# Performance work log

Measured on AMD Instinct MI355X. Metric: run time of the kernel, lower is better.

## Reference

```python
import jax, jax.numpy as jnp
import numpy as np

B, L, D = 8, 8192, 1024
M = L // 4  # target_ratio=4 -> exactly L/4 boundaries per batch row (enforced in setup_inputs)


@jax.custom_vjp
def ste(x):
    # Forward: ones_like(x). Backward: pass gradient straight through.
    return jnp.ones_like(x)

def _ste_fwd(x):
    return jnp.ones_like(x), None

def _ste_bwd(_, g):
    return (g,)

ste.defvjp(_ste_fwd, _ste_bwd)


def _ema_combine(c1, c2):
    # Linear recurrence h = a*h_prev + b as an associative op (matches the
    # Hillis-Steele doubling scan in the torch source exactly).
    a1, b1 = c1
    a2, b2 = c2
    return (a1 * a2, a2[..., None] * b1 + b2)


def setup_inputs() -> dict:
    key = jax.random.key(0)
    k1, k2, k3, k4, k5 = jax.random.split(key, 5)
    x = jax.random.normal(k1, (B, L, D), jnp.float32)
    residual = jax.random.normal(k2, (B, L, D), jnp.float32)
    prob = jax.random.uniform(k3, (B, L), jnp.float32)
    # exactly M=L//4 True positions per row (random locations) -> static M
    r = jax.random.uniform(k4, (B, L))
    sel = jnp.argsort(r, axis=1)[:, :M]
    token_mask = jnp.zeros((B, L), bool).at[jnp.arange(B)[:, None], sel].set(True)
    state = jax.random.normal(k5, (B, D), jnp.float32)
    return {"x": x, "residual": residual, "prob": prob,
            "token_mask": token_mask, "state": state}


def reference(x, residual, prob, token_mask, state):
    # ---- Tokenizer: compact selected positions to the front (stable order) ----
    counts = token_mask.sum(axis=1)                       # (B,)
    order = jnp.argsort(~token_mask, axis=1)[:, :M]       # stable: True positions first, in order
    chunked = jnp.take_along_axis(x, order[:, :, None], axis=1)      # (B, M, D)
    chunk_probs = jnp.take_along_axis(prob, order, axis=1)           # (B, M)
    valid = jnp.arange(M)[None, :] < counts[:, None]                  # (B, M)
    chunk_probs = chunk_probs * valid                     # padded slots -> 0 (new_zeros semantics)

    # ---- EMA scan over compacted chunks ----
    decay = jnp.clip(1.0 - chunk_probs, 0.0, 1.0)         # (B, M)
    b = (1.0 - decay)[..., None] * chunked                # (B, M, D)
    b = b.at[:, 0].add(decay[:, 0, None] * state)         # fold initial state into b[0]
    _, ema = jax.lax.associative_scan(_ema_combine, (decay, b), axis=1)
    ema = ema * valid[..., None]

    # ---- DeTokenizer: scatter-expand back to (B, L, D) ----
    chunk_idx = jnp.cumsum(token_mask.astype(jnp.int32), axis=1) - 1  # (B, L)
    valid_pos = chunk_idx >= 0
    ci = jnp.clip(chunk_idx, 0, M - 1)
    long_states = jnp.take_along_axis(ema, ci[:, :, None], axis=1)    # (B, L, D)
    long_states = long_states * valid_pos[..., None]

    coef = ste(jnp.maximum(1.0 - prob, prob))             # forward: ones; bwd: STE
    long_states = long_states * coef[..., None]

    output = residual + long_states                       # (B, L, D)

    # new_state = last valid EMA value per batch (or carried-over state if empty)
    last = jnp.clip(counts - 1, 0, M - 1)
    new_state = jnp.take_along_axis(ema, last[:, None, None], axis=1)[:, 0]
    new_state = jnp.where((counts > 0)[:, None], new_state, state)
    return output, new_state
```

## Files before the change

kernel.cpp:

```cpp
#include <hip/hip_runtime.h>
#include <stdint.h>
#include <stddef.h>

#define B_ 8
#define L_ 8192
#define D_ 1024
#define M_ 2048
#define S_ 128
#define G_ 16
#define D4_ (D_/4)
#define TROWS_ 64
#define NTILE_ (L_/TROWS_)

typedef float f4 __attribute__((ext_vector_type(4)));

#define OFF_POS    ((size_t)0)
#define OFF_DEC    (OFF_POS  + (size_t)B_*M_*4)
#define OFF_A      (OFF_DEC  + (size_t)B_*M_*4)
#define OFF_CIT    (OFF_A    + (size_t)B_*S_*4)
#define OFF_EZ     (OFF_CIT  + (size_t)B_*NTILE_*4)
#define OFF_HINIT  (OFF_EZ   + (size_t)B_*S_*D_*4)
#define WS_TOTAL   (OFF_HINIT + (size_t)B_*S_*D_*4)

__global__ __launch_bounds__(1024)
void compact_kernel(const void* __restrict__ mask_raw,
                    const float* __restrict__ prob,
                    int* __restrict__ pos,
                    float* __restrict__ dec,
                    int* __restrict__ ci_tile) {
    const int b = blockIdx.x;
    const int t = threadIdx.x;

    __shared__ int u8flag;
    if (t == 0) u8flag = 0;
    __syncthreads();
    {
        const uint32_t* mu = (const uint32_t*)mask_raw;
        uint32_t w0 = mu[t * 2], w1 = mu[t * 2 + 1];
        if (w0 > 1u || w1 > 1u) atomicOr(&u8flag, 1);
    }
    __syncthreads();
    const bool u8 = (u8flag != 0);

    int mv[8];
    const int base_l = t * 8;
    if (u8) {
        const uint8_t* mrow = (const uint8_t*)mask_raw + (size_t)b * L_;
        #pragma unroll
        for (int j = 0; j < 8; j++) mv[j] = mrow[base_l + j] ? 1 : 0;
    } else {
        const int* mrow = (const int*)mask_raw + (size_t)b * L_;
        #pragma unroll
        for (int j = 0; j < 8; j++) mv[j] = mrow[base_l + j] ? 1 : 0;
    }
    int tsum = 0;
    #pragma unroll
    for (int j = 0; j < 8; j++) tsum += mv[j];

    const int lane = t & 63, wid = t >> 6;
    int v = tsum;
    #pragma unroll
    for (int off = 1; off < 64; off <<= 1) {
        int n = __shfl_up(v, off, 64);
        if (lane >= off) v += n;
    }
    __shared__ int wsum[16];
    __shared__ int woff[16];
    if (lane == 63) wsum[wid] = v;
    __syncthreads();
    if (t < 16) {
        int acc = 0;
        for (int w = 0; w < t; w++) acc += wsum[w];
        woff[t] = acc;
    }
    __syncthreads();
    int run = (v - tsum) + woff[wid];

    const float* prow = prob + (size_t)b * L_;
    #pragma unroll
    for (int j = 0; j < 8; j++) {
        const int l = base_l + j;
        if (mv[j]) {
            float d = 1.0f - prow[l];
            d = fminf(fmaxf(d, 0.0f), 1.0f);
            pos[(size_t)b * M_ + run] = l;
            dec[(size_t)b * M_ + run] = d;
            run += 1;
        }
    }
    if ((t & 7) == 7) {
        const int k = (t + 1) >> 3;
        if (k < NTILE_) ci_tile[b * NTILE_ + k] = run - 1;
    }
}

__global__ __launch_bounds__(256)
void segend_kernel(const f4* __restrict__ x4,
                   const int* __restrict__ pos,
                   const float* __restrict__ dec,
                   f4* __restrict__ ez4,
                   float* __restrict__ Aseg) {
    const int blk = blockIdx.x;
    const int b = blk / S_, s = blk % S_;
    const int t = threadIdx.x;
    __shared__ int   pl[G_];
    __shared__ float dl[G_];
    if (t < G_) {
        pl[t] = pos[(size_t)b * M_ + (size_t)s * G_ + t];
        dl[t] = dec[(size_t)b * M_ + (size_t)s * G_ + t];
    }
    __syncthreads();
    f4 h = (f4)(0.0f);
    #pragma unroll
    for (int m = 0; m < G_; m++) {
        const float d = dl[m];
        h = d * h + (1.0f - d) * x4[((size_t)b * L_ + pl[m]) * D4_ + t];
    }
    ez4[(size_t)blk * D4_ + t] = h;
    if (t == 0) {
        float p = 1.0f;
        #pragma unroll
        for (int m = 0; m < G_; m++) p *= dl[m];
        Aseg[blk] = p;
    }
}

__global__ __launch_bounds__(64)
void combine_kernel(const float* __restrict__ ez,
                    const float* __restrict__ Aseg,
                    const float* __restrict__ state,
                    float* __restrict__ hinit,
                    float* __restrict__ newstate) {
    const int b = blockIdx.x;
    const int ch = blockIdx.y * 64 + threadIdx.x;
    __shared__ float Al[S_];
    for (int i = threadIdx.x; i < S_; i += 64) Al[i] = Aseg[b * S_ + i];
    __syncthreads();

    float c = state[(size_t)b * D_ + ch];
    for (int s0 = 0; s0 < S_; s0 += 8) {
        float e[8];
        #pragma unroll
        for (int j = 0; j < 8; j++)
            e[j] = ez[((size_t)b * S_ + s0 + j) * D_ + ch];
        #pragma unroll
        for (int j = 0; j < 8; j++) {
            hinit[((size_t)b * S_ + s0 + j) * D_ + ch] = c;
            c = fmaf(Al[s0 + j], c, e[j]);
        }
    }
    newstate[(size_t)b * D_ + ch] = c;
}

__global__ __launch_bounds__(256)
void fused_kernel(const f4* __restrict__ x4,
                  const f4* __restrict__ res4,
                  const int* __restrict__ pos,
                  const float* __restrict__ dec,
                  const int* __restrict__ ci_tile,
                  const float* __restrict__ state,
                  const f4* __restrict__ hinit4,
                  f4* __restrict__ out4) {
    const int blk = blockIdx.x;
    const int b = blk >> 7;
    const int k = blk & (NTILE_ - 1);
    const int t = threadIdx.x;
    const int l0 = k * TROWS_;

    const int m0 = (k == 0) ? -1 : ci_tile[b * NTILE_ + k];

    __shared__ int   pl[TROWS_ + 2];
    __shared__ float dl[TROWS_ + 2];
    if (t < TROWS_ + 2) {
        const int mm = m0 + 1 + t;
        if (mm < M_) {
            pl[t] = pos[(size_t)b * M_ + mm];
            dl[t] = dec[(size_t)b * M_ + mm];
        } else {
            pl[t] = L_;
            dl[t] = 1.0f;
        }
    }
    __syncthreads();

    const f4* xrow = x4 + (size_t)b * L_ * D4_;

    f4 h;
    float live;
    if (m0 < 0) {
        h = ((const f4*)state)[(size_t)b * D4_ + t];
        live = 0.0f;
    } else {
        const int s0 = m0 >> 4;
        const int mbase = s0 << 4;
        h = hinit4[((size_t)b * S_ + s0) * D4_ + t];
        live = 1.0f;
        #pragma unroll
        for (int j = 0; j < G_; j++) {
            const int mj = mbase + j;
            const float draw = dec[(size_t)b * M_ + mj];
            const float d = (mj <= m0) ? draw : 1.0f;
            const f4 xv = xrow[(size_t)pos[(size_t)b * M_ + mj] * D4_ + t];
            h = d * h + (1.0f - d) * xv;
        }
    }

    const f4* resrow = res4 + (size_t)b * L_ * D4_;
    f4*       outrow = out4 + (size_t)b * L_ * D4_;

    int mi = 0;
    int nextb = pl[0];
    int a0 = (pl[0] < L_) ? pl[0] : 0;
    int a1 = (pl[1] < L_) ? pl[1] : 0;
    f4 xn  = xrow[(size_t)a0 * D4_ + t];
    f4 xn2 = xrow[(size_t)a1 * D4_ + t];
    int l = l0;

    #define ADV(K, HH, LV)                                                \
        if (l + (K) == nextb) {                                           \
            const float d_ = dl[mi];                                      \
            h = d_ * h + (1.0f - d_) * xn;                                \
            live = 1.0f;                                                  \
            xn = xn2;                                                     \
            ++mi;                                                         \
            nextb = pl[mi];                                               \
            const int nr_ = (pl[mi + 1] < L_) ? pl[mi + 1] : 0;           \
            xn2 = xrow[(size_t)nr_ * D4_ + t];                            \
        }                                                                 \
        HH = h; LV = live;

    f4 c0, c1, c2, c3;
    c0 = __builtin_nontemporal_load(resrow + (size_t)(l + 0) * D4_ + t);
    c1 = __builtin_nontemporal_load(resrow + (size_t)(l + 1) * D4_ + t);
    c2 = __builtin_nontemporal_load(resrow + (size_t)(l + 2) * D4_ + t);
    c3 = __builtin_nontemporal_load(resrow + (size_t)(l + 3) * D4_ + t);
    for (int g = 0; g < (TROWS_ / 4) - 1; ++g) {
        f4 n0 = __builtin_nontemporal_load(resrow + (size_t)(l + 4) * D4_ + t);
        f4 n1 = __builtin_nontemporal_load(resrow + (size_t)(l + 5) * D4_ + t);
        f4 n2 = __builtin_nontemporal_load(resrow + (size_t)(l + 6) * D4_ + t);
        f4 n3 = __builtin_nontemporal_load(resrow + (size_t)(l + 7) * D4_ + t);
        f4 h0, h1, h2, h3;
        float v0, v1, v2, v3;
        ADV(0, h0, v0); ADV(1, h1, v1); ADV(2, h2, v2); ADV(3, h3, v3);
        __builtin_nontemporal_store(c0 + v0 * h0, outrow + (size_t)(l + 0) * D4_ + t);
        __builtin_nontemporal_store(c1 + v1 * h1, outrow + (size_t)(l + 1) * D4_ + t);
        __builtin_nontemporal_store(c2 + v2 * h2, outrow + (size_t)(l + 2) * D4_ + t);
        __builtin_nontemporal_store(c3 + v3 * h3, outrow + (size_t)(l + 3) * D4_ + t);
        c0 = n0; c1 = n1; c2 = n2; c3 = n3;
        l += 4;
    }
    {
        f4 h0, h1, h2, h3;
        float v0, v1, v2, v3;
        ADV(0, h0, v0); ADV(1, h1, v1); ADV(2, h2, v2); ADV(3, h3, v3);
        __builtin_nontemporal_store(c0 + v0 * h0, outrow + (size_t)(l + 0) * D4_ + t);
        __builtin_nontemporal_store(c1 + v1 * h1, outrow + (size_t)(l + 1) * D4_ + t);
        __builtin_nontemporal_store(c2 + v2 * h2, outrow + (size_t)(l + 2) * D4_ + t);
        __builtin_nontemporal_store(c3 + v3 * h3, outrow + (size_t)(l + 3) * D4_ + t);
    }
    #undef ADV
}

extern "C" void kernel_launch(void* const* d_in, const int* in_sizes, int n_in,
                              void* d_out, int out_size, void* d_ws, size_t ws_size,
                              hipStream_t stream) {
    const float* x        = (const float*)d_in[0];
    const float* residual = (const float*)d_in[1];
    const float* prob     = (const float*)d_in[2];
    const void*  mask     = d_in[3];
    const float* state    = (const float*)d_in[4];

    float* out       = (float*)d_out;
    float* new_state = out + (size_t)B_ * L_ * D_;

    if (ws_size < WS_TOTAL) return;

    char* ws = (char*)d_ws;
    int*   pos     = (int*)  (ws + OFF_POS);
    float* dec     = (float*)(ws + OFF_DEC);
    float* Aseg    = (float*)(ws + OFF_A);
    int*   ci_tile = (int*)  (ws + OFF_CIT);
    float* ez      = (float*)(ws + OFF_EZ);
    float* hinit   = (float*)(ws + OFF_HINIT);

    compact_kernel<<<B_, 1024, 0, stream>>>(mask, prob, pos, dec, ci_tile);

    segend_kernel<<<B_ * S_, 256, 0, stream>>>(
        (const f4*)x, pos, dec, (f4*)ez, Aseg);

    combine_kernel<<<dim3(B_, 16), 64, 0, stream>>>(
        ez, Aseg, state, hinit, new_state);

    fused_kernel<<<B_ * NTILE_, 256, 0, stream>>>(
        (const f4*)x, (const f4*)residual, pos, dec, ci_tile, state,
        (const f4*)hinit, (f4*)out);
}
```

Baseline: 140.0 us.

## Align EMA segment boundaries with output tiles to drop per-tile prefix recompute

Scan segments are now defined by the output tiles (64 rows each) rather than fixed 16-chunk groups. Each segend block reduces exactly the chunks that fall inside its tile, and combine produces a per-tile initial state. The fused kernel then loads its starting state directly instead of replaying up to 16 gathered x rows. The catch is variable-length segments (load imbalance when a tile holds many boundaries), a per-tile ez/hinit workspace of the same size, and a padding gather of row 0 when a segment's count is not a multiple of 8.

```diff
diff --git a/kernel.cpp b/kernel.cpp
--- a/kernel.cpp
+++ b/kernel.cpp
@@ -6,8 +6,6 @@
 #define L_ 8192
 #define D_ 1024
 #define M_ 2048
-#define S_ 128
-#define G_ 16
 #define D4_ (D_/4)
 #define TROWS_ 64
 #define NTILE_ (L_/TROWS_)
@@ -17,10 +15,10 @@
 #define OFF_POS    ((size_t)0)
 #define OFF_DEC    (OFF_POS  + (size_t)B_*M_*4)
 #define OFF_A      (OFF_DEC  + (size_t)B_*M_*4)
-#define OFF_CIT    (OFF_A    + (size_t)B_*S_*4)
+#define OFF_CIT    (OFF_A    + (size_t)B_*NTILE_*4)
 #define OFF_EZ     (OFF_CIT  + (size_t)B_*NTILE_*4)
-#define OFF_HINIT  (OFF_EZ   + (size_t)B_*S_*D_*4)
-#define WS_TOTAL   (OFF_HINIT + (size_t)B_*S_*D_*4)
+#define OFF_HINIT  (OFF_EZ   + (size_t)B_*NTILE_*D_*4)
+#define WS_TOTAL   (OFF_HINIT + (size_t)B_*NTILE_*D_*4)
 
 __global__ __launch_bounds__(1024)
 void compact_kernel(const void* __restrict__ mask_raw,
@@ -98,31 +96,49 @@
 void segend_kernel(const f4* __restrict__ x4,
                    const int* __restrict__ pos,
                    const float* __restrict__ dec,
+                   const int* __restrict__ ci_tile,
                    f4* __restrict__ ez4,
                    float* __restrict__ Aseg) {
     const int blk = blockIdx.x;
-    const int b = blk / S_, s = blk % S_;
+    const int b = blk >> 7;
+    const int k = blk & (NTILE_ - 1);
     const int t = threadIdx.x;
-    __shared__ int   pl[G_];
-    __shared__ float dl[G_];
-    if (t < G_) {
-        pl[t] = pos[(size_t)b * M_ + (size_t)s * G_ + t];
-        dl[t] = dec[(size_t)b * M_ + (size_t)s * G_ + t];
-    }
-    __syncthreads();
+
+    const int mlo = (k == 0) ? 0 : ci_tile[b * NTILE_ + k] + 1;
+    const int mhi = (k == NTILE_ - 1) ? (M_ - 1) : ci_tile[b * NTILE_ + k + 1];
+    const int n = mhi - mlo + 1;
+
+    __shared__ int   pl[TROWS_];
+    __shared__ float dl[TROWS_];
+    if (t < n) {
+        pl[t] = pos[(size_t)b * M_ + mlo + t];
+        dl[t] = dec[(size_t)b * M_ + mlo + t];
+    }
+    __syncthreads();
+
     f4 h = (f4)(0.0f);
-    #pragma unroll
-    for (int m = 0; m < G_; m++) {
-        const float d = dl[m];
-        h = d * h + (1.0f - d) * x4[((size_t)b * L_ + pl[m]) * D4_ + t];
+    float A = 1.0f;
+    if (n > 0) {
+        const f4* xrow = x4 + (size_t)b * L_ * D4_;
+        for (int g = 0; g < n; g += 8) {
+            f4    xv[8];
+            float dd[8];
+            #pragma unroll
+            for (int j = 0; j < 8; j++) {
+                const int mm = g + j;
+                const int mc = (mm < n) ? mm : 0;
+                dd[j] = (mm < n) ? dl[mc] : 1.0f;
+                xv[j] = xrow[(size_t)pl[mc] * D4_ + t];
+            }
+            #pragma unroll
+            for (int j = 0; j < 8; j++) {
+                h = dd[j] * h + (1.0f - dd[j]) * xv[j];
+                A *= dd[j];
+            }
+        }
     }
     ez4[(size_t)blk * D4_ + t] = h;
-    if (t == 0) {
-        float p = 1.0f;
-        #pragma unroll
-        for (int m = 0; m < G_; m++) p *= dl[m];
-        Aseg[blk] = p;
-    }
+    if (t == 0) Aseg[blk] = A;
 }
 
 __global__ __launch_bounds__(64)
@@ -133,19 +149,19 @@
                     float* __restrict__ newstate) {
     const int b = blockIdx.x;
     const int ch = blockIdx.y * 64 + threadIdx.x;
-    __shared__ float Al[S_];
-    for (int i = threadIdx.x; i < S_; i += 64) Al[i] = Aseg[b * S_ + i];
+    __shared__ float Al[NTILE_];
+    for (int i = threadIdx.x; i < NTILE_; i += 64) Al[i] = Aseg[b * NTILE_ + i];
     __syncthreads();
 
     float c = state[(size_t)b * D_ + ch];
-    for (int s0 = 0; s0 < S_; s0 += 8) {
+    for (int s0 = 0; s0 < NTILE_; s0 += 8) {
         float e[8];
         #pragma unroll
         for (int j = 0; j < 8; j++)
-            e[j] = ez[((size_t)b * S_ + s0 + j) * D_ + ch];
+            e[j] = ez[((size_t)b * NTILE_ + s0 + j) * D_ + ch];
         #pragma unroll
         for (int j = 0; j < 8; j++) {
-            hinit[((size_t)b * S_ + s0 + j) * D_ + ch] = c;
+            hinit[((size_t)b * NTILE_ + s0 + j) * D_ + ch] = c;
             c = fmaf(Al[s0 + j], c, e[j]);
         }
     }
@@ -158,7 +174,6 @@
                   const int* __restrict__ pos,
                   const float* __restrict__ dec,
                   const int* __restrict__ ci_tile,
-                  const float* __restrict__ state,
                   const f4* __restrict__ hinit4,
                   f4* __restrict__ out4) {
     const int blk = blockIdx.x;
@@ -185,25 +200,8 @@
 
     const f4* xrow = x4 + (size_t)b * L_ * D4_;
 
-    f4 h;
-    float live;
-    if (m0 < 0) {
-        h = ((const f4*)state)[(size_t)b * D4_ + t];
-        live = 0.0f;
-    } else {
-        const int s0 = m0 >> 4;
-        const int mbase = s0 << 4;
-        h = hinit4[((size_t)b * S_ + s0) * D4_ + t];
-        live = 1.0f;
-        #pragma unroll
-        for (int j = 0; j < G_; j++) {
-            const int mj = mbase + j;
-            const float draw = dec[(size_t)b * M_ + mj];
-            const float d = (mj <= m0) ? draw : 1.0f;
-            const f4 xv = xrow[(size_t)pos[(size_t)b * M_ + mj] * D4_ + t];
-            h = d * h + (1.0f - d) * xv;
-        }
-    }
+    f4 h = hinit4[(size_t)blk * D4_ + t];
+    float live = (m0 >= 0) ? 1.0f : 0.0f;
 
     const f4* resrow = res4 + (size_t)b * L_ * D4_;
     f4*       outrow = out4 + (size_t)b * L_ * D4_;
@@ -285,13 +283,13 @@
 
     compact_kernel<<<B_, 1024, 0, stream>>>(mask, prob, pos, dec, ci_tile);
 
-    segend_kernel<<<B_ * S_, 256, 0, stream>>>(
-        (const f4*)x, pos, dec, (f4*)ez, Aseg);
+    segend_kernel<<<B_ * NTILE_, 256, 0, stream>>>(
+        (const f4*)x, pos, dec, ci_tile, (f4*)ez, Aseg);
 
     combine_kernel<<<dim3(B_, 16), 64, 0, stream>>>(
         ez, Aseg, state, hinit, new_state);
 
     fused_kernel<<<B_ * NTILE_, 256, 0, stream>>>(
-        (const f4*)x, (const f4*)residual, pos, dec, ci_tile, state,
+        (const f4*)x, (const f4*)residual, pos, dec, ci_tile,
         (const f4*)hinit, (f4*)out);
 }
```

New measurement: 134.9 us. -3.6%, faster.
